# Kernel tuning notes

Hardware: AMD Instinct MI355X
Metric: run time of the kernel (lower is better)

The kernel has to match this reference:

```python
import jax, jax.numpy as jnp
import numpy as np
import math

F, H, N_CURR = 16384, 64, 8192
BOUNDARY = -0.01


def setup_inputs() -> dict:
    key = jax.random.key(0)
    ks = jax.random.split(key, 12)
    he_w = math.sqrt(2.0 / (H + 1))
    he_t = math.sqrt(2.0)
    return {
        "X": jax.random.normal(ks[0], (F,), jnp.float32),
        "delta": jax.random.uniform(ks[1], (F,), jnp.float32),
        "Ht": jax.random.normal(ks[2], (F, H), jnp.float32),
        "c_t": jax.random.normal(ks[3], (H,), jnp.float32),
        "c_global": jax.random.normal(ks[4], (F, H), jnp.float32),
        "lstm_weights": he_w * jax.random.normal(ks[5], (F, 3 * H, H + 1), jnp.float32),
        "lstm_bias": jnp.zeros((F, 3 * H), jnp.float32),
        "lstm_xT_weights": he_t * jax.random.normal(ks[6], (F, 2 * H, 1), jnp.float32),
        "lstm_xT_bias": jnp.zeros((F, 2 * H), jnp.float32),
        "lstm_delT_weights": he_t * jax.random.normal(ks[7], (F, 3 * H, 1), jnp.float32),
        "lstm_c_inp_weights": jax.random.normal(ks[8], (F, H), jnp.float32),
        "lstm_c_out_weights": jax.random.normal(ks[9], (F, H), jnp.float32),
        "feat_idx": jnp.arange(N_CURR, dtype=jnp.int32),
    }


def reference(X, delta, Ht, c_t, c_global, lstm_weights, lstm_bias,
              lstm_xT_weights, lstm_xT_bias, lstm_delT_weights,
              lstm_c_inp_weights, lstm_c_out_weights, feat_idx):
    # weight constraint on the hidden_size-th row of delT weights (clip to <= boundary)
    delT_w = lstm_delT_weights.at[:, H, :].set(
        jnp.minimum(lstm_delT_weights[:, H, :], BOUNDARY))

    x = X[feat_idx]                                   # [n]
    h_prev = Ht[feat_idx]                             # [n, H]
    cur_input = jnp.concatenate([x[:, None], h_prev], axis=-1)   # [n, H+1]

    # gathered per-feature small matvecs
    cur_out = jnp.einsum('ngh,nh->ng', lstm_weights[feat_idx], cur_input) \
        + lstm_bias[feat_idx]                          # [n, 3H]
    xm_out = lstm_xT_weights[feat_idx, :, 0] * x[:, None] + lstm_xT_bias[feat_idx]   # [n, 2H]
    dT_out = delT_w[feat_idx, :, 0] * delta[feat_idx][:, None]                        # [n, 3H]

    gate_input, gate_output, gate_pre_c = jnp.split(cur_out, 3, axis=-1)
    xm_T1, xm_T2 = jnp.split(xm_out, 2, axis=-1)
    del_T1, del_T2, del_To = jnp.split(dT_out, 3, axis=-1)

    T_1t = jax.nn.sigmoid(xm_T1 + jax.nn.sigmoid(del_T1))
    T_2t = jax.nn.sigmoid(xm_T2 + jax.nn.sigmoid(del_T2))
    gate_input = jax.nn.sigmoid(gate_input + lstm_c_inp_weights[feat_idx] * c_t)
    gate_pre_c = jnp.tanh(gate_pre_c)

    c_tilde = (1.0 - gate_input * T_1t) * c_t + gate_input * T_1t * gate_pre_c
    c_new = (1.0 - gate_input) * c_t + gate_input * T_2t * gate_pre_c
    gate_output = jax.nn.sigmoid(
        gate_output + lstm_c_out_weights[feat_idx] * c_tilde + del_To)

    h_new = gate_output * jnp.tanh(c_tilde)            # [n, H]

    H_curr = jnp.zeros_like(Ht).at[feat_idx].set(h_new)     # scatter into [F, H]
    c_global_new = c_global.at[feat_idx].set(c_new)
    C_curr = jnp.mean(c_new, axis=0)                   # aggregate_by='Mean' -> [H]
    return H_curr, c_global_new, C_curr
```

## Files before the change

### kernel.cpp

```cpp
#include <hip/hip_runtime.h>
#include <cstdint>
#include <cstddef>

#define HH 64
#define G3 192
#define G2 128
#define ROW 12480
#define BOUNDARY (-0.01f)

__device__ __forceinline__ float sigm(float x) { return 1.0f / (1.0f + __expf(-x)); }

__device__ __forceinline__ void load_lds16(const float* g, float* l) {
    __builtin_amdgcn_global_load_lds(
        (const __attribute__((address_space(1))) void*)g,
        (__attribute__((address_space(3))) void*)l,
        16, 0, 0);
}

__global__ __launch_bounds__(256) void init_kernel(float* __restrict__ outH,
                                                   float* __restrict__ outC,
                                                   const float* __restrict__ c_global,
                                                   int fh4) {
    int idx = blockIdx.x * 256 + threadIdx.x;
    int stride = gridDim.x * 256;
    for (int k = idx; k < fh4; k += stride) {
        ((float4*)outH)[k] = make_float4(0.f, 0.f, 0.f, 0.f);
        ((float4*)outC)[k] = ((const float4*)c_global)[k];
    }
}

__global__ __launch_bounds__(256) void lstm_main(
    const float* __restrict__ X, const float* __restrict__ delta,
    const float* __restrict__ Ht, const float* __restrict__ c_t,
    const float* __restrict__ W, const float* __restrict__ bias,
    const float* __restrict__ xTw, const float* __restrict__ xTb,
    const float* __restrict__ dTw, const float* __restrict__ cinw,
    const float* __restrict__ coutw, const int* __restrict__ feat_idx,
    float* __restrict__ outH, float* __restrict__ outC) {

    __shared__ float w[ROW];
    __shared__ float inp[72];
    __shared__ float co[G3];

    const int t = threadIdx.x;
    const int i = feat_idx[blockIdx.x];
    const int wave = t >> 6;
    const int lane = t & 63;

    if (t == 0) inp[0] = X[i];
    if (wave == 1) inp[1 + lane] = Ht[(size_t)i * HH + lane];

    const float* wrow = W + (size_t)i * ROW;
    for (int c = wave; c < 49; c += 4) {
        int fbase = c * 256;
        int fidx = fbase + lane * 4;
        if (fidx < ROW) load_lds16(wrow + fidx, &w[fbase]);
    }
    __syncthreads();

    if (t < G3) {
        const float* wr = &w[t * 65];
        float acc = bias[(size_t)i * G3 + t];
        #pragma unroll
        for (int h = 0; h < 65; ++h) acc = fmaf(wr[h], inp[h], acc);
        co[t] = acc;
    }
    __syncthreads();

    if (t < HH) {
        const float xi = inp[0];
        const float di = delta[i];
        const float ct = c_t[t];
        const size_t i1 = (size_t)i * HH;
        const size_t i2 = (size_t)i * G2;
        const size_t i3 = (size_t)i * G3;

        float gi_pre = co[t];
        float go_pre = co[HH + t];
        float gc = tanhf(co[2 * HH + t]);

        float xm1 = fmaf(xTw[i2 + t], xi, xTb[i2 + t]);
        float xm2 = fmaf(xTw[i2 + HH + t], xi, xTb[i2 + HH + t]);

        float dw1 = dTw[i3 + t];
        float dw2 = dTw[i3 + HH + t];
        if (t == 0) dw2 = fminf(dw2, BOUNDARY);
        float dwo = dTw[i3 + 2 * HH + t];

        float T1 = sigm(xm1 + sigm(dw1 * di));
        float T2 = sigm(xm2 + sigm(dw2 * di));
        float gi = sigm(gi_pre + cinw[i1 + t] * ct);

        float gT1 = gi * T1;
        float c_tilde = (1.f - gT1) * ct + gT1 * gc;
        float c_new = (1.f - gi) * ct + gi * T2 * gc;
        float go = sigm(go_pre + coutw[i1 + t] * c_tilde + dwo * di);
        float h_new = go * tanhf(c_tilde);

        outH[i1 + t] = h_new;
        outC[i1 + t] = c_new;
    }
}

__global__ __launch_bounds__(256) void reduceA(const float* __restrict__ outC,
                                               const int* __restrict__ feat_idx,
                                               float* __restrict__ partial, int n) {
    __shared__ float s[256];
    const int b = blockIdx.x, t = threadIdx.x;
    const int h = t & 63, g = t >> 6;
    const int rend = min(n, (b + 1) * 32);
    float acc = 0.f;
    for (int r = b * 32 + g; r < rend; r += 4)
        acc += outC[(size_t)feat_idx[r] * HH + h];
    s[t] = acc;
    __syncthreads();
    if (t < HH) partial[b * HH + h] = s[h] + s[64 + h] + s[128 + h] + s[192 + h];
}

__global__ __launch_bounds__(256) void reduceB(const float* __restrict__ partial,
                                               float* __restrict__ outM,
                                               int nblocks, int n) {
    __shared__ float s[256];
    const int t = threadIdx.x, h = t & 63, g = t >> 6;
    float acc = 0.f;
    for (int b = g; b < nblocks; b += 4) acc += partial[(size_t)b * HH + h];
    s[t] = acc;
    __syncthreads();
    if (t < HH) outM[h] = (s[h] + s[64 + h] + s[128 + h] + s[192 + h]) / (float)n;
}

__global__ __launch_bounds__(256) void reduceAll(const float* __restrict__ outC,
                                                 const int* __restrict__ feat_idx,
                                                 float* __restrict__ outM, int n) {
    __shared__ float s[256];
    const int t = threadIdx.x, h = t & 63, g = t >> 6;
    float acc = 0.f;
    for (int r = g; r < n; r += 4)
        acc += outC[(size_t)feat_idx[r] * HH + h];
    s[t] = acc;
    __syncthreads();
    if (t < HH) outM[h] = (s[h] + s[64 + h] + s[128 + h] + s[192 + h]) / (float)n;
}

extern "C" void kernel_launch(void* const* d_in, const int* in_sizes, int n_in,
                              void* d_out, int out_size, void* d_ws, size_t ws_size,
                              hipStream_t stream) {
    const float* X        = (const float*)d_in[0];
    const float* delta    = (const float*)d_in[1];
    const float* Ht       = (const float*)d_in[2];
    const float* c_t      = (const float*)d_in[3];
    const float* c_global = (const float*)d_in[4];
    const float* W        = (const float*)d_in[5];
    const float* bias     = (const float*)d_in[6];
    const float* xTw      = (const float*)d_in[7];
    const float* xTb      = (const float*)d_in[8];
    const float* dTw      = (const float*)d_in[9];
    const float* cinw     = (const float*)d_in[10];
    const float* coutw    = (const float*)d_in[11];
    const int*   feat_idx = (const int*)d_in[12];

    const int F  = in_sizes[0];
    const int n  = in_sizes[12];
    const int FH = F * HH;

    float* out  = (float*)d_out;
    float* outH = out;
    float* outC = out + FH;
    float* outM = out + 2 * FH;

    {
        int fh4 = FH / 4;
        int blocks = (fh4 + 255) / 256;
        if (blocks > 2048) blocks = 2048;
        init_kernel<<<blocks, 256, 0, stream>>>(outH, outC, c_global, fh4);
    }

    lstm_main<<<n, 256, 0, stream>>>(X, delta, Ht, c_t, W, bias, xTw, xTb,
                                     dTw, cinw, coutw, feat_idx, outH, outC);

    int nA = (n + 31) / 32;
    if (ws_size >= (size_t)nA * HH * sizeof(float)) {
        float* partial = (float*)d_ws;
        reduceA<<<nA, 256, 0, stream>>>(outC, feat_idx, partial, n);
        reduceB<<<1, 256, 0, stream>>>(partial, outM, nA, n);
    } else {
        reduceAll<<<1, 256, 0, stream>>>(outC, feat_idx, outM, n);
    }
}
```

Baseline: 112.2 us.

## Split each feature across two blocks by hidden half to cut LDS per block

The main LSTM kernel now launches two blocks per feature, each handling 32 of the 64 hidden units. Each block loads only its third of the weight rows into LDS (about 25 KB instead of 50 KB), which is meant to raise occupancy and memory-level parallelism. Per-feature side loads (gate weights, biases, c_t) are issued up front, before the weight load barrier, so their latency overlaps the weight fetch. Small vectors (the input and Ht row) are now loaded twice, once per block, and the first reduction uses 128 rows per block instead of 32.

```diff
diff --git a/kernel.cpp b/kernel.cpp
--- a/kernel.cpp
+++ b/kernel.cpp
@@ -5,7 +5,8 @@
 #define HH 64
 #define G3 192
 #define G2 128
-#define ROW 12480
+#define ROWF 12480
+#define CHF 2080
 #define BOUNDARY (-0.01f)
 
 __device__ __forceinline__ float sigm(float x) { return 1.0f / (1.0f + __expf(-x)); }
@@ -38,67 +39,90 @@
     const float* __restrict__ coutw, const int* __restrict__ feat_idx,
     float* __restrict__ outH, float* __restrict__ outC) {
 
-    __shared__ float w[ROW];
+    __shared__ float w[3 * CHF];
     __shared__ float inp[72];
-    __shared__ float co[G3];
-
-    const int t = threadIdx.x;
-    const int i = feat_idx[blockIdx.x];
-    const int wave = t >> 6;
+    __shared__ float co[96];
+
+    const int t    = threadIdx.x;
+    const int b    = blockIdx.x;
+    const int f    = b >> 1;
+    const int hb   = (b & 1) << 5;
+    const int i    = feat_idx[f];
     const int lane = t & 63;
+    const int wv   = t >> 6;
+
+    const size_t i1 = (size_t)i * HH;
+    const size_t i2 = (size_t)i * G2;
+    const size_t i3 = (size_t)i * G3;
+
+    float xi = 0.f, di = 0.f, ct = 0.f, cinv = 0.f, coutv = 0.f;
+    float xw1 = 0.f, xw2 = 0.f, xb1 = 0.f, xb2 = 0.f;
+    float dw1 = 0.f, dw2 = 0.f, dwo = 0.f, bv = 0.f;
+    if (t < 32) {
+        const int h = hb + t;
+        xi   = X[i];
+        di   = delta[i];
+        ct   = c_t[h];
+        cinv = cinw[i1 + h];
+        coutv = coutw[i1 + h];
+        xw1  = xTw[i2 + h];
+        xw2  = xTw[i2 + HH + h];
+        xb1  = xTb[i2 + h];
+        xb2  = xTb[i2 + HH + h];
+        dw1  = dTw[i3 + h];
+        dw2  = dTw[i3 + HH + h];
+        dwo  = dTw[i3 + 2 * HH + h];
+    }
+    if (t < 96) {
+        const int ch = t >> 5, idx = t & 31;
+        bv = bias[i3 + ch * HH + hb + idx];
+    }
 
     if (t == 0) inp[0] = X[i];
-    if (wave == 1) inp[1 + lane] = Ht[(size_t)i * HH + lane];
-
-    const float* wrow = W + (size_t)i * ROW;
-    for (int c = wave; c < 49; c += 4) {
-        int fbase = c * 256;
-        int fidx = fbase + lane * 4;
-        if (fidx < ROW) load_lds16(wrow + fidx, &w[fbase]);
-    }
-    __syncthreads();
-
-    if (t < G3) {
-        const float* wr = &w[t * 65];
-        float acc = bias[(size_t)i * G3 + t];
+    if (wv == 1) inp[1 + lane] = Ht[i1 + lane];
+
+    const float* wrow = W + (size_t)i * ROWF;
+    for (int s = wv; s < 27; s += 4) {
+        const int ch  = s / 9;
+        const int off = s % 9;
+        const int fl  = off * 256 + lane * 4;
+        if (fl < CHF)
+            load_lds16(wrow + (size_t)(64 * ch + hb) * 65 + fl,
+                       &w[ch * CHF + off * 256]);
+    }
+    __syncthreads();
+
+    if (t < 96) {
+        const int ch = t >> 5, idx = t & 31;
+        const float* wr = &w[ch * CHF + idx * 65];
+        float acc = bv;
         #pragma unroll
-        for (int h = 0; h < 65; ++h) acc = fmaf(wr[h], inp[h], acc);
+        for (int k = 0; k < 65; ++k) acc = fmaf(wr[k], inp[k], acc);
         co[t] = acc;
     }
     __syncthreads();
 
-    if (t < HH) {
-        const float xi = inp[0];
-        const float di = delta[i];
-        const float ct = c_t[t];
-        const size_t i1 = (size_t)i * HH;
-        const size_t i2 = (size_t)i * G2;
-        const size_t i3 = (size_t)i * G3;
-
+    if (t < 32) {
+        const int h = hb + t;
         float gi_pre = co[t];
-        float go_pre = co[HH + t];
-        float gc = tanhf(co[2 * HH + t]);
-
-        float xm1 = fmaf(xTw[i2 + t], xi, xTb[i2 + t]);
-        float xm2 = fmaf(xTw[i2 + HH + t], xi, xTb[i2 + HH + t]);
-
-        float dw1 = dTw[i3 + t];
-        float dw2 = dTw[i3 + HH + t];
-        if (t == 0) dw2 = fminf(dw2, BOUNDARY);
-        float dwo = dTw[i3 + 2 * HH + t];
+        float go_pre = co[32 + t];
+        float gc     = tanhf(co[64 + t]);
+
+        float xm1 = fmaf(xw1, xi, xb1);
+        float xm2 = fmaf(xw2, xi, xb2);
+        if (h == 0) dw2 = fminf(dw2, BOUNDARY);
 
         float T1 = sigm(xm1 + sigm(dw1 * di));
         float T2 = sigm(xm2 + sigm(dw2 * di));
-        float gi = sigm(gi_pre + cinw[i1 + t] * ct);
-
-        float gT1 = gi * T1;
+        float gi = sigm(gi_pre + cinv * ct);
+
+        float gT1     = gi * T1;
         float c_tilde = (1.f - gT1) * ct + gT1 * gc;
-        float c_new = (1.f - gi) * ct + gi * T2 * gc;
-        float go = sigm(go_pre + coutw[i1 + t] * c_tilde + dwo * di);
-        float h_new = go * tanhf(c_tilde);
-
-        outH[i1 + t] = h_new;
-        outC[i1 + t] = c_new;
+        float c_new   = (1.f - gi) * ct + gi * T2 * gc;
+        float go      = sigm(go_pre + coutv * c_tilde + dwo * di);
+
+        outH[i1 + h] = go * tanhf(c_tilde);
+        outC[i1 + h] = c_new;
     }
 }
 
@@ -108,9 +132,9 @@
     __shared__ float s[256];
     const int b = blockIdx.x, t = threadIdx.x;
     const int h = t & 63, g = t >> 6;
-    const int rend = min(n, (b + 1) * 32);
+    const int rend = min(n, (b + 1) * 128);
     float acc = 0.f;
-    for (int r = b * 32 + g; r < rend; r += 4)
+    for (int r = b * 128 + g; r < rend; r += 4)
         acc += outC[(size_t)feat_idx[r] * HH + h];
     s[t] = acc;
     __syncthreads();
@@ -175,10 +199,10 @@
         init_kernel<<<blocks, 256, 0, stream>>>(outH, outC, c_global, fh4);
     }
 
-    lstm_main<<<n, 256, 0, stream>>>(X, delta, Ht, c_t, W, bias, xTw, xTb,
-                                     dTw, cinw, coutw, feat_idx, outH, outC);
-
-    int nA = (n + 31) / 32;
+    lstm_main<<<2 * n, 256, 0, stream>>>(X, delta, Ht, c_t, W, bias, xTw, xTb,
+                                         dTw, cinw, coutw, feat_idx, outH, outC);
+
+    int nA = (n + 127) / 128;
     if (ws_size >= (size_t)nA * HH * sizeof(float)) {
         float* partial = (float*)d_ws;
         reduceA<<<nA, 256, 0, stream>>>(outC, feat_idx, partial, n);
```

Result: no change. 110.6 us (-1.4%).

## Stream LSTM weights directly from global with 16-lane shuffle-reduced matvec

Applied to the files above, without the earlier changes.

Drops the LDS staging of each feature's 12480-float weight row. The 192x65 matvec now runs from global memory, with 16 lanes per output row: each lane takes strided columns and the partial sums are combined with xor shuffles. All 256 threads take part instead of 192. The per-feature parameter loads are hoisted before the first barrier so their latency overlaps the input staging. The mean reduction also uses 64 rows per block instead of 32. Global loads are now strided by 16 floats per lane within a row, so coalescing is weaker. In exchange, LDS use drops from about 50KB per block, which allows higher occupancy.

```diff
diff --git a/kernel.cpp b/kernel.cpp
--- a/kernel.cpp
+++ b/kernel.cpp
@@ -3,19 +3,13 @@
 #include <cstddef>
 
 #define HH 64
+#define G2 128
 #define G3 192
-#define G2 128
-#define ROW 12480
+#define WROW 65
+#define ROWF 12480
 #define BOUNDARY (-0.01f)
 
 __device__ __forceinline__ float sigm(float x) { return 1.0f / (1.0f + __expf(-x)); }
-
-__device__ __forceinline__ void load_lds16(const float* g, float* l) {
-    __builtin_amdgcn_global_load_lds(
-        (const __attribute__((address_space(1))) void*)g,
-        (__attribute__((address_space(3))) void*)l,
-        16, 0, 0);
-}
 
 __global__ __launch_bounds__(256) void init_kernel(float* __restrict__ outH,
                                                    float* __restrict__ outC,
@@ -38,66 +32,72 @@
     const float* __restrict__ coutw, const int* __restrict__ feat_idx,
     float* __restrict__ outH, float* __restrict__ outC) {
 
-    __shared__ float w[ROW];
-    __shared__ float inp[72];
+    __shared__ __align__(16) float inp[68];
     __shared__ float co[G3];
 
     const int t = threadIdx.x;
     const int i = feat_idx[blockIdx.x];
-    const int wave = t >> 6;
-    const int lane = t & 63;
+    const size_t i1 = (size_t)i * HH;
+    const size_t i2 = (size_t)i * G2;
+    const size_t i3 = (size_t)i * G3;
+
+    float xi = 0.f, di = 0.f, ct = 0.f, cinv = 0.f, coutv = 0.f;
+    float xw1 = 0.f, xw2 = 0.f, xb1 = 0.f, xb2 = 0.f;
+    float dw1 = 0.f, dw2 = 0.f, dwo = 0.f, b0 = 0.f, b1 = 0.f, b2 = 0.f;
+    if (t < HH) {
+        xi = X[i];  di = delta[i];  ct = c_t[t];
+        cinv = cinw[i1 + t];  coutv = coutw[i1 + t];
+        xw1 = xTw[i2 + t];  xw2 = xTw[i2 + HH + t];
+        xb1 = xTb[i2 + t];  xb2 = xTb[i2 + HH + t];
+        dw1 = dTw[i3 + t];  dw2 = dTw[i3 + HH + t];  dwo = dTw[i3 + 2 * HH + t];
+        b0 = bias[i3 + t];  b1 = bias[i3 + HH + t];  b2 = bias[i3 + 2 * HH + t];
+    }
 
     if (t == 0) inp[0] = X[i];
-    if (wave == 1) inp[1 + lane] = Ht[(size_t)i * HH + lane];
-
-    const float* wrow = W + (size_t)i * ROW;
-    for (int c = wave; c < 49; c += 4) {
-        int fbase = c * 256;
-        int fidx = fbase + lane * 4;
-        if (fidx < ROW) load_lds16(wrow + fidx, &w[fbase]);
-    }
+    if (t >= 64 && t < 128) inp[1 + (t - 64)] = Ht[i1 + (t - 64)];
     __syncthreads();
 
-    if (t < G3) {
-        const float* wr = &w[t * 65];
-        float acc = bias[(size_t)i * G3 + t];
-        #pragma unroll
-        for (int h = 0; h < 65; ++h) acc = fmaf(wr[h], inp[h], acc);
-        co[t] = acc;
+    {
+        const int G = t >> 4, j = t & 15;
+        const float in0 = inp[j], in1 = inp[j + 16], in2 = inp[j + 32], in3 = inp[j + 48];
+        const float in4 = inp[64];
+        const float* wp = W + (size_t)i * ROWF + G * WROW + j;
+        #pragma unroll 4
+        for (int k = 0; k < 12; ++k) {
+            const float* wr = wp + k * (16 * WROW);
+            float acc = wr[0] * in0;
+            acc = fmaf(wr[16], in1, acc);
+            acc = fmaf(wr[32], in2, acc);
+            acc = fmaf(wr[48], in3, acc);
+            if (j == 0) acc = fmaf(wr[64 - j], in4, acc);
+            acc += __shfl_xor(acc, 1);
+            acc += __shfl_xor(acc, 2);
+            acc += __shfl_xor(acc, 4);
+            acc += __shfl_xor(acc, 8);
+            if (j == 0) co[G + 16 * k] = acc;
+        }
     }
     __syncthreads();
 
     if (t < HH) {
-        const float xi = inp[0];
-        const float di = delta[i];
-        const float ct = c_t[t];
-        const size_t i1 = (size_t)i * HH;
-        const size_t i2 = (size_t)i * G2;
-        const size_t i3 = (size_t)i * G3;
+        float gi_pre = co[t] + b0;
+        float go_pre = co[HH + t] + b1;
+        float gc     = tanhf(co[2 * HH + t] + b2);
 
-        float gi_pre = co[t];
-        float go_pre = co[HH + t];
-        float gc = tanhf(co[2 * HH + t]);
-
-        float xm1 = fmaf(xTw[i2 + t], xi, xTb[i2 + t]);
-        float xm2 = fmaf(xTw[i2 + HH + t], xi, xTb[i2 + HH + t]);
-
-        float dw1 = dTw[i3 + t];
-        float dw2 = dTw[i3 + HH + t];
+        float xm1 = fmaf(xw1, xi, xb1);
+        float xm2 = fmaf(xw2, xi, xb2);
         if (t == 0) dw2 = fminf(dw2, BOUNDARY);
-        float dwo = dTw[i3 + 2 * HH + t];
 
         float T1 = sigm(xm1 + sigm(dw1 * di));
         float T2 = sigm(xm2 + sigm(dw2 * di));
-        float gi = sigm(gi_pre + cinw[i1 + t] * ct);
+        float gi = sigm(gi_pre + cinv * ct);
 
-        float gT1 = gi * T1;
+        float gT1     = gi * T1;
         float c_tilde = (1.f - gT1) * ct + gT1 * gc;
-        float c_new = (1.f - gi) * ct + gi * T2 * gc;
-        float go = sigm(go_pre + coutw[i1 + t] * c_tilde + dwo * di);
-        float h_new = go * tanhf(c_tilde);
+        float c_new   = (1.f - gi) * ct + gi * T2 * gc;
+        float go      = sigm(go_pre + coutv * c_tilde + dwo * di);
 
-        outH[i1 + t] = h_new;
+        outH[i1 + t] = go * tanhf(c_tilde);
         outC[i1 + t] = c_new;
     }
 }
@@ -108,9 +108,9 @@
     __shared__ float s[256];
     const int b = blockIdx.x, t = threadIdx.x;
     const int h = t & 63, g = t >> 6;
-    const int rend = min(n, (b + 1) * 32);
+    const int rend = min(n, (b + 1) * 64);
     float acc = 0.f;
-    for (int r = b * 32 + g; r < rend; r += 4)
+    for (int r = b * 64 + g; r < rend; r += 4)
         acc += outC[(size_t)feat_idx[r] * HH + h];
     s[t] = acc;
     __syncthreads();
@@ -178,7 +178,7 @@
     lstm_main<<<n, 256, 0, stream>>>(X, delta, Ht, c_t, W, bias, xTw, xTb,
                                      dTw, cinw, coutw, feat_idx, outH, outC);
 
-    int nA = (n + 31) / 32;
+    int nA = (n + 63) / 64;
     if (ws_size >= (size_t)nA * HH * sizeof(float)) {
         float* partial = (float*)d_ws;
         reduceA<<<nA, 256, 0, stream>>>(outC, feat_idx, partial, n);
```

Result: slower. 117.7 us (+4.9%).
